# Kernel optimization log

Hardware: AMD Instinct MI355X
Metric: run time of the kernel (lower is better)

## Reference

```python
import jax, jax.numpy as jnp
import numpy as np

TOP_K = 2
N_EXPERTS = 8
N_EMBED = 1024
B, T = 4, 1024


def setup_inputs() -> dict:
    key = jax.random.key(0)
    k1, k2, k3 = jax.random.split(key, 3)
    x = jax.random.normal(k1, (B, T, N_EMBED), dtype=jnp.float32)
    wg_kernel = jax.random.normal(k2, (N_EMBED, N_EXPERTS), dtype=jnp.float32) * 0.02
    wg_bias = jnp.zeros((N_EXPERTS,), dtype=jnp.float32)
    # Experts.__call__ only uses w_c_fc: (E, C, C), stddev 0.02
    w_c_fc = jax.random.normal(k3, (N_EXPERTS, N_EMBED, N_EMBED), dtype=jnp.float32) * 0.02
    return {"x": x, "wg_kernel": wg_kernel, "wg_bias": wg_bias, "w_c_fc": w_c_fc}


def _dispatch(xb, logits, n_experts, top_k):
    # xb: (T, C), logits: (T, E)
    T, C = xb.shape
    top_k_logits, idx = jax.lax.top_k(logits, top_k)          # (T, k)
    probs = jax.nn.softmax(top_k_logits, axis=-1)             # (T, k)
    flat_idx = jnp.swapaxes(idx, 0, 1).ravel()                # (k*T,), k-major order
    one_hot = jax.nn.one_hot(flat_idx, n_experts, dtype=jnp.int32)
    pos = jnp.cumsum(one_hot, axis=0) * one_hot - 1           # running slot per expert
    pos = jnp.swapaxes(pos.reshape(top_k, T, n_experts), 0, 1).max(axis=2)  # (T, k)
    idx_tk = jnp.swapaxes(flat_idx.reshape(top_k, T), 0, 1)   # (T, k)
    cap = top_k * T
    x_rep = jnp.repeat(xb, top_k, axis=0)                     # (T*k, C), token-major
    buf = jnp.zeros((n_experts, cap, C), xb.dtype)
    buf = buf.at[idx_tk.ravel(), pos.ravel()].add(x_rep)      # scatter dispatch
    return probs, pos, idx_tk, buf


def reference(x, wg_kernel, wg_bias, w_c_fc):
    Bb, Tt, C = x.shape
    n_experts = w_c_fc.shape[0]
    logits = x @ wg_kernel + wg_bias                           # (B, T, E)
    probs, pos, idx, buf = jax.vmap(
        lambda xb, lb: _dispatch(xb, lb, n_experts, TOP_K))(x, logits)
    # buf: (B, E, cap, C). The original's reshape/swapaxes shuffle is a pure
    # permutation of the (B, cap) token axis that is exactly inverted after the
    # expert GEMM, so it is mathematically a no-op; apply the grouped GEMM directly.
    out = jnp.einsum('beti,eio->beto', buf, w_c_fc)            # per-expert matmul
    gathered = jax.vmap(lambda o, i, p: o[i, p])(out, idx, pos)  # (B, T, k, C)
    y = jnp.einsum('btkc,btk->btc', gathered, probs)
    return y, probs
```

## Files before the change

kernel.cpp:

```cpp
#include <hip/hip_runtime.h>
#include <math.h>

typedef __attribute__((ext_vector_type(8))) __bf16 bf16x8;
typedef __attribute__((ext_vector_type(4))) __bf16 bf16x4v;
typedef __attribute__((ext_vector_type(16))) float f32x16;

#define N_TOK  4096
#define C_DIM  1024
#define N_EXP  8
#define CAP    4096

#define WS_CNT    0
#define WS_PERM   32768
#define WS_XB     ((size_t)1 << 20)
#define WS_WT     (WS_XB + ((size_t)8 << 20))

#define GLD16(g, l)                                                        \
  __builtin_amdgcn_global_load_lds(                                        \
      (const __attribute__((address_space(1))) void*)(g),                  \
      (__attribute__((address_space(3))) void*)(l), 16, 0, 0)

__global__ __launch_bounds__(256)
void prep_kernel(const float* __restrict__ x, const float* __restrict__ wg,
                 const float* __restrict__ bias, const float* __restrict__ W,
                 __bf16* __restrict__ xb, float* __restrict__ probs,
                 __bf16* __restrict__ Wt, int* __restrict__ cnt,
                 int* __restrict__ perm) {
  __shared__ __align__(16) char smem[32768];
  __shared__ int lcnt[N_EXP], base[N_EXP];
  const int tid = threadIdx.x;

  if (blockIdx.x < 256) {
    float (*wgT)[C_DIM] = (float (*)[C_DIM])smem;
    if (tid < N_EXP) lcnt[tid] = 0;

#pragma unroll
    for (int i = 0; i < 8; ++i) {
      const float4 v = ((const float4*)wg)[i * 256 + tid];
      const int f = (i * 256 + tid) * 4;
      const int c = f >> 3;
      const int e = f & 7;
      wgT[e][c] = v.x; wgT[e + 1][c] = v.y; wgT[e + 2][c] = v.z; wgT[e + 3][c] = v.w;
    }
    __syncthreads();

    const int lane = tid & 63;
    const int wv   = tid >> 6;
    int re0[4], re1[4], rs0[4], rs1[4];

#pragma unroll
    for (int s = 0; s < 4; ++s) {
      const int t = blockIdx.x * 16 + wv * 4 + s;
      const float4* xrow = (const float4*)(x + (size_t)t * C_DIM);
      float acc[N_EXP];
#pragma unroll
      for (int e = 0; e < N_EXP; ++e) acc[e] = 0.f;

#pragma unroll
      for (int j = 0; j < 4; ++j) {
        const int c4 = j * 64 + lane;
        const float4 v = xrow[c4];
        bf16x4v bv = { (__bf16)v.x, (__bf16)v.y, (__bf16)v.z, (__bf16)v.w };
        *(bf16x4v*)(xb + (size_t)t * C_DIM + c4 * 4) = bv;
#pragma unroll
        for (int e = 0; e < N_EXP; ++e) {
          const float4 w = *(const float4*)&wgT[e][c4 * 4];
          acc[e] += v.x * w.x + v.y * w.y + v.z * w.z + v.w * w.w;
        }
      }

#pragma unroll
      for (int off = 32; off >= 1; off >>= 1) {
#pragma unroll
        for (int e = 0; e < N_EXP; ++e) acc[e] += __shfl_xor(acc[e], off, 64);
      }

      if (lane == 0) {
        float l[N_EXP];
#pragma unroll
        for (int e = 0; e < N_EXP; ++e) l[e] = acc[e] + bias[e];
        int e0 = 0;
#pragma unroll
        for (int e = 1; e < N_EXP; ++e) if (l[e] > l[e0]) e0 = e;
        int e1 = (e0 == 0) ? 1 : 0;
#pragma unroll
        for (int e = 0; e < N_EXP; ++e) if (e != e0 && l[e] > l[e1]) e1 = e;
        const float p0 = 1.f / (1.f + expf(l[e1] - l[e0]));
        probs[t * 2]     = p0;
        probs[t * 2 + 1] = 1.f - p0;
        re0[s] = e0; re1[s] = e1;
        rs0[s] = atomicAdd(&lcnt[e0], 1);
        rs1[s] = atomicAdd(&lcnt[e1], 1);
      }
    }
    __syncthreads();
    if (tid < N_EXP) base[tid] = atomicAdd(&cnt[tid], lcnt[tid]);
    __syncthreads();
    if (lane == 0) {
#pragma unroll
      for (int s = 0; s < 4; ++s) {
        const int t = blockIdx.x * 16 + wv * 4 + s;
        perm[re0[s] * CAP + base[re0[s]] + rs0[s]] = t * 2;
        perm[re1[s] * CAP + base[re1[s]] + rs1[s]] = t * 2 + 1;
      }
    }
  } else {
    __bf16 (*tile)[33] = (__bf16 (*)[33])smem;
    const int b  = blockIdx.x - 256;
    const int e  = b >> 10;
    const int r  = b & 1023;
    const int i0 = (r >> 5) * 32;
    const int o0 = (r & 31) * 32;
    const float* We  = W  + (size_t)e * C_DIM * C_DIM;
    __bf16*      Wte = Wt + (size_t)e * C_DIM * C_DIM;
    const int tx = tid & 31, ty = tid >> 5;
#pragma unroll
    for (int j = 0; j < 32; j += 8)
      tile[ty + j][tx] = (__bf16)We[(size_t)(i0 + ty + j) * C_DIM + o0 + tx];
    __syncthreads();
#pragma unroll
    for (int j = 0; j < 32; j += 8)
      Wte[(size_t)(o0 + ty + j) * C_DIM + i0 + tx] = tile[tx][ty + j];
  }
}

__global__ __launch_bounds__(256)
void moe_gemm(const __bf16* __restrict__ xb, const __bf16* __restrict__ Wt,
              const int* __restrict__ cnt, const int* __restrict__ perm,
              __bf16* __restrict__ buf) {
  const int gid = blockIdx.x;
  const int e   = gid & 7;
  const int n0  = ((gid >> 3) & 7) * 128;
  const int m0  = (gid >> 6) * 64;
  const int count = cnt[e];
  if (m0 >= count) return;

  const int*    permE = perm + e * CAP;
  const __bf16* We    = Wt + (size_t)e * C_DIM * C_DIM;

  __shared__ char AsB[8192];
  __shared__ char BsB[16384];

  const int tid  = threadIdx.x;
  const int lane = tid & 63;
  const int wv   = tid >> 6;
  const int wr = wv >> 1, wc = wv & 1;
  const int l32 = lane & 31, hi = lane >> 5;

  const int rsub  = lane >> 3;
  const int chunk = (lane & 7) ^ rsub;
  int tk[2];
#pragma unroll
  for (int q = 0; q < 2; ++q) {
    const int i = m0 + wv * 16 + q * 8 + rsub;
    tk[q] = (i < count) ? (permE[i] >> 1) : 0;
  }
  const char* gB = (const char*)We + (size_t)(n0 + wv * 32 + rsub) * 2048 + chunk * 16;
  char* ldsA = AsB + wv * 2048;
  char* ldsB = BsB + wv * 4096;

  f32x16 acc[2];
#pragma unroll
  for (int ng = 0; ng < 2; ++ng)
#pragma unroll
    for (int r = 0; r < 16; ++r) acc[ng][r] = 0.f;

  for (int kt = 0; kt < 16; ++kt) {
    const int kb = kt * 128;
#pragma unroll
    for (int q = 0; q < 2; ++q)
      GLD16((const char*)xb + (size_t)tk[q] * 2048 + kb + chunk * 16,
            ldsA + q * 1024);
#pragma unroll
    for (int q = 0; q < 4; ++q)
      GLD16(gB + (size_t)q * 8 * 2048 + kb, ldsB + q * 1024);
    __syncthreads();

#pragma unroll
    for (int ks = 0; ks < 4; ++ks) {
      const int c = ks * 2 + hi;
      const int rA = wr * 32 + l32;
      const bf16x8 af = *(const bf16x8*)(AsB + rA * 128 + ((c ^ (rA & 7)) << 4));
      bf16x8 bfr[2];
#pragma unroll
      for (int ng = 0; ng < 2; ++ng) {
        const int rB = wc * 64 + ng * 32 + l32;
        bfr[ng] = *(const bf16x8*)(BsB + rB * 128 + ((c ^ (rB & 7)) << 4));
      }
#pragma unroll
      for (int ng = 0; ng < 2; ++ng)
        acc[ng] = __builtin_amdgcn_mfma_f32_32x32x16_bf16(af, bfr[ng], acc[ng], 0, 0, 0);
    }
    __syncthreads();
  }

#pragma unroll
  for (int r = 0; r < 16; ++r) {
    const int row = (r & 3) + 8 * (r >> 2) + 4 * hi;
    const int i = m0 + wr * 32 + row;
    if (i < count) {
      const int pe = permE[i];
      __bf16* orow = buf + (size_t)(pe >> 1) * 2048 + (pe & 1) * 1024 +
                     n0 + wc * 64 + l32;
      orow[0]  = (__bf16)acc[0][r];
      orow[32] = (__bf16)acc[1][r];
    }
  }
}

__global__ __launch_bounds__(256)
void combine(const float* __restrict__ probs, float* __restrict__ y) {
  const int t = blockIdx.x;
  const int c = threadIdx.x * 4;
  const __bf16* bt = (const __bf16*)(y + (size_t)t * C_DIM);
  const bf16x4v b0 = *(const bf16x4v*)(bt + c);
  const bf16x4v b1 = *(const bf16x4v*)(bt + 1024 + c);
  const float p0 = probs[2 * t], p1 = probs[2 * t + 1];
  __syncthreads();
  float4 o = { p0 * (float)b0[0] + p1 * (float)b1[0],
               p0 * (float)b0[1] + p1 * (float)b1[1],
               p0 * (float)b0[2] + p1 * (float)b1[2],
               p0 * (float)b0[3] + p1 * (float)b1[3] };
  *(float4*)(y + (size_t)t * C_DIM + c) = o;
}

extern "C" void kernel_launch(void* const* d_in, const int* in_sizes, int n_in,
                              void* d_out, int out_size, void* d_ws, size_t ws_size,
                              hipStream_t stream) {
  const float* x    = (const float*)d_in[0];
  const float* wg   = (const float*)d_in[1];
  const float* bias = (const float*)d_in[2];
  const float* wcfc = (const float*)d_in[3];

  float* y     = (float*)d_out;
  float* probs = y + (size_t)N_TOK * C_DIM;
  __bf16* buf  = (__bf16*)d_out;

  char* ws   = (char*)d_ws;
  int*    cnt  = (int*)(ws + WS_CNT);
  int*    perm = (int*)(ws + WS_PERM);
  __bf16* xb   = (__bf16*)(ws + WS_XB);
  __bf16* Wt   = (__bf16*)(ws + WS_WT);

  hipMemsetAsync(cnt, 0, N_EXP * sizeof(int), stream);

  prep_kernel<<<256 + 8192, 256, 0, stream>>>(x, wg, bias, wcfc, xb, probs,
                                              Wt, cnt, perm);
  moe_gemm<<<8 * 8 * 64, 256, 0, stream>>>(xb, Wt, cnt, perm, buf);
  combine<<<N_TOK, 256, 0, stream>>>(probs, y);
}
```

Measured before the change: 135.7 us.

## Restructure MoE GEMM to two waves with 64x64 per-wave tiles using 16x16x32 MFMA

The grouped expert GEMM drops from four waves per block to two. Each wave now computes a 64x64 output sub-tile with a 4x4 grid of 16x16x32 bf16 MFMAs instead of a 32x64 tile with 32x32x16 MFMAs. This raises fragment reuse from LDS, with each A and B fragment feeding four MFMAs, and changes the global-to-LDS load split across threads. The cost is more accumulator registers per thread and half as many threads per block to hide load latency, partly offset by a launch-bounds hint asking for four blocks per CU.

```diff
diff --git a/kernel.cpp b/kernel.cpp
--- a/kernel.cpp
+++ b/kernel.cpp
@@ -3,7 +3,7 @@
 
 typedef __attribute__((ext_vector_type(8))) __bf16 bf16x8;
 typedef __attribute__((ext_vector_type(4))) __bf16 bf16x4v;
-typedef __attribute__((ext_vector_type(16))) float f32x16;
+typedef __attribute__((ext_vector_type(4))) float f32x4;
 
 #define N_TOK  4096
 #define C_DIM  1024
@@ -124,7 +124,7 @@
   }
 }
 
-__global__ __launch_bounds__(256)
+__global__ __launch_bounds__(128, 4)
 void moe_gemm(const __bf16* __restrict__ xb, const __bf16* __restrict__ Wt,
               const int* __restrict__ cnt, const int* __restrict__ perm,
               __bf16* __restrict__ buf) {
@@ -144,66 +144,77 @@
   const int tid  = threadIdx.x;
   const int lane = tid & 63;
   const int wv   = tid >> 6;
-  const int wr = wv >> 1, wc = wv & 1;
-  const int l32 = lane & 31, hi = lane >> 5;
-
-  const int rsub  = lane >> 3;
-  const int chunk = (lane & 7) ^ rsub;
-  int tk[2];
-#pragma unroll
-  for (int q = 0; q < 2; ++q) {
-    const int i = m0 + wv * 16 + q * 8 + rsub;
+  const int nw   = wv * 64;
+  const int l16 = lane & 15, quad = lane >> 4;
+
+  const int rsub  = tid >> 3;
+  const int chunk = (tid & 7) ^ (rsub & 7);
+  int tk[4];
+#pragma unroll
+  for (int q = 0; q < 4; ++q) {
+    const int i = m0 + q * 16 + rsub;
     tk[q] = (i < count) ? (permE[i] >> 1) : 0;
   }
-  const char* gB = (const char*)We + (size_t)(n0 + wv * 32 + rsub) * 2048 + chunk * 16;
-  char* ldsA = AsB + wv * 2048;
-  char* ldsB = BsB + wv * 4096;
-
-  f32x16 acc[2];
-#pragma unroll
-  for (int ng = 0; ng < 2; ++ng)
-#pragma unroll
-    for (int r = 0; r < 16; ++r) acc[ng][r] = 0.f;
+  const char* gB = (const char*)We + (size_t)(n0 + rsub) * 2048 + chunk * 16;
+  char* ldsA = AsB + wv * 1024;
+  char* ldsB = BsB + wv * 1024;
+
+  f32x4 acc[4][4];
+  const f32x4 zero = {0.f, 0.f, 0.f, 0.f};
+#pragma unroll
+  for (int mi = 0; mi < 4; ++mi)
+#pragma unroll
+    for (int ni = 0; ni < 4; ++ni) acc[mi][ni] = zero;
 
   for (int kt = 0; kt < 16; ++kt) {
     const int kb = kt * 128;
 #pragma unroll
-    for (int q = 0; q < 2; ++q)
+    for (int q = 0; q < 4; ++q)
       GLD16((const char*)xb + (size_t)tk[q] * 2048 + kb + chunk * 16,
-            ldsA + q * 1024);
-#pragma unroll
-    for (int q = 0; q < 4; ++q)
-      GLD16(gB + (size_t)q * 8 * 2048 + kb, ldsB + q * 1024);
-    __syncthreads();
-
-#pragma unroll
-    for (int ks = 0; ks < 4; ++ks) {
-      const int c = ks * 2 + hi;
-      const int rA = wr * 32 + l32;
-      const bf16x8 af = *(const bf16x8*)(AsB + rA * 128 + ((c ^ (rA & 7)) << 4));
-      bf16x8 bfr[2];
-#pragma unroll
-      for (int ng = 0; ng < 2; ++ng) {
-        const int rB = wc * 64 + ng * 32 + l32;
-        bfr[ng] = *(const bf16x8*)(BsB + rB * 128 + ((c ^ (rB & 7)) << 4));
-      }
-#pragma unroll
-      for (int ng = 0; ng < 2; ++ng)
-        acc[ng] = __builtin_amdgcn_mfma_f32_32x32x16_bf16(af, bfr[ng], acc[ng], 0, 0, 0);
-    }
-    __syncthreads();
-  }
-
-#pragma unroll
-  for (int r = 0; r < 16; ++r) {
-    const int row = (r & 3) + 8 * (r >> 2) + 4 * hi;
-    const int i = m0 + wr * 32 + row;
-    if (i < count) {
-      const int pe = permE[i];
-      __bf16* orow = buf + (size_t)(pe >> 1) * 2048 + (pe & 1) * 1024 +
-                     n0 + wc * 64 + l32;
-      orow[0]  = (__bf16)acc[0][r];
-      orow[32] = (__bf16)acc[1][r];
+            ldsA + q * 2048);
+#pragma unroll
+    for (int q = 0; q < 8; ++q)
+      GLD16(gB + (size_t)q * 16 * 2048 + kb, ldsB + q * 2048);
+    __syncthreads();
+
+#pragma unroll
+    for (int ks = 0; ks < 2; ++ks) {
+      bf16x8 af[4], bfr[4];
+#pragma unroll
+      for (int mi = 0; mi < 4; ++mi) {
+        const int rA = mi * 16 + l16;
+        af[mi] = *(const bf16x8*)(AsB + rA * 128 +
+                                  (((ks * 4 + quad) ^ (rA & 7)) << 4));
+      }
+#pragma unroll
+      for (int ni = 0; ni < 4; ++ni) {
+        const int rB = nw + ni * 16 + l16;
+        bfr[ni] = *(const bf16x8*)(BsB + rB * 128 +
+                                   (((ks * 4 + quad) ^ (rB & 7)) << 4));
+      }
+#pragma unroll
+      for (int mi = 0; mi < 4; ++mi)
+#pragma unroll
+        for (int ni = 0; ni < 4; ++ni)
+          acc[mi][ni] = __builtin_amdgcn_mfma_f32_16x16x32_bf16(
+              af[mi], bfr[ni], acc[mi][ni], 0, 0, 0);
+    }
+    __syncthreads();
+  }
+
+#pragma unroll
+  for (int mi = 0; mi < 4; ++mi) {
+#pragma unroll
+    for (int r = 0; r < 4; ++r) {
+      const int i = m0 + mi * 16 + quad * 4 + r;
+      if (i < count) {
+        const int pe = permE[i];
+        __bf16* orow = buf + (size_t)(pe >> 1) * 2048 + (pe & 1) * 1024 +
+                       n0 + nw + l16;
+#pragma unroll
+        for (int ni = 0; ni < 4; ++ni)
+          orow[ni * 16] = (__bf16)acc[mi][ni][r];
+      }
     }
   }
 }
@@ -246,6 +257,6 @@
 
   prep_kernel<<<256 + 8192, 256, 0, stream>>>(x, wg, bias, wcfc, xb, probs,
                                               Wt, cnt, perm);
-  moe_gemm<<<8 * 8 * 64, 256, 0, stream>>>(xb, Wt, cnt, perm, buf);
+  moe_gemm<<<8 * 8 * 64, 128, 0, stream>>>(xb, Wt, cnt, perm, buf);
   combine<<<N_TOK, 256, 0, stream>>>(probs, y);
 }
```

Measured after the change: 147.4 us. +8.6%, slower.
